# Kernel optimization log

Hardware: AMD Instinct MI355X
Metric: run time of the kernel (lower is better)

## Reference

```python
import jax, jax.numpy as jnp
import numpy as np

NEAR, FAR, N_SAMPLES = 1.0, 6.0, 64
FAR_APPEND = 1000.0


def setup_inputs() -> dict:
    key = jax.random.key(0)
    ks = jax.random.split(key, 8)
    B, R = 2, 4096
    # pixel coords in a 128x128 image
    x_pix = jax.random.uniform(ks[0], (B, R, 2), dtype=jnp.float32) * 128.0
    # plausible pinhole intrinsics (fx=fy=128, cx=cy=64)
    K = jnp.array([[128.0, 0.0, 64.0], [0.0, 128.0, 64.0], [0.0, 0.0, 1.0]], dtype=jnp.float32)
    intrinsics = jnp.tile(K[None], (B, 1, 1))
    # identity rotation, small translation cam2world
    c2w = jnp.eye(4, dtype=jnp.float32).at[:3, 3].set(jnp.array([0.1, -0.2, 0.5]))
    cam2world = jnp.tile(c2w[None], (B, 1, 1))
    H = 256
    W1 = jax.random.normal(ks[1], (3, H), dtype=jnp.float32) / np.sqrt(3.0)
    b1 = jnp.zeros((H,), jnp.float32)
    W2 = jax.random.normal(ks[2], (H, H), dtype=jnp.float32) / np.sqrt(H)
    b2 = jnp.zeros((H,), jnp.float32)
    W3 = jax.random.normal(ks[3], (H, 4), dtype=jnp.float32) / np.sqrt(H)
    b3 = jnp.zeros((4,), jnp.float32)
    return {"x_pix": x_pix, "intrinsics": intrinsics, "cam2world": cam2world,
            "W1": W1, "b1": b1, "W2": W2, "b2": b2, "W3": W3, "b3": b3}


def _radiance_field(pts, W1, b1, W2, b2, W3, b3):
    # pts: (B, N, 3) -> sigma (B, N, 1), rad (B, N, 3)
    h = jax.nn.relu(pts @ W1 + b1)
    h = jax.nn.relu(h @ W2 + b2)
    o = h @ W3 + b3
    return jax.nn.relu(o[..., :1]), jax.nn.sigmoid(o[..., 1:])


def _get_world_rays(x_pix, intrinsics, cam2world):
    B, R, _ = x_pix.shape
    inv_K = jnp.linalg.inv(intrinsics)  # (B,3,3)
    xy_hom = jnp.concatenate([x_pix, jnp.ones((B, R, 1), x_pix.dtype)], axis=-1)  # (B,R,3)
    dirs_cam = jnp.einsum("bij,brj->bri", inv_K, xy_hom)  # unnormalized cam-frame dirs
    dirs_hom = jnp.concatenate([dirs_cam, jnp.zeros((B, R, 1), x_pix.dtype)], axis=-1)  # w=0 vector
    dirs_world = jnp.einsum("bij,brj->bri", cam2world, dirs_hom)[..., :3]
    origins = jnp.broadcast_to(cam2world[:, None, :3, 3], (B, R, 3))
    return origins, dirs_world


def _volume_integral(z_vals, sigmas, radiances):
    # z_vals: (S,); sigmas: (B,R,S,1); radiances: (B,R,S,3)
    dists = jnp.diff(z_vals, append=jnp.array([FAR_APPEND], z_vals.dtype))  # (S,)
    alpha = 1.0 - jnp.exp(-sigmas * dists[None, None, :, None])  # (B,R,S,1)
    Ts = jnp.cumprod(1.0 - alpha, axis=2)  # inclusive cumprod, matching torch
    weights = alpha * Ts  # (B,R,S,1)
    rgb = jnp.sum(weights * radiances, axis=2)  # (B,R,3)
    depth_map = jnp.einsum("brsv,s->brv", weights, z_vals)  # (B,R,1)
    return rgb, depth_map, weights


def reference(x_pix, intrinsics, cam2world, W1, b1, W2, b2, W3, b3):
    B, R = x_pix.shape[0], x_pix.shape[1]
    ros, rds = _get_world_rays(x_pix, intrinsics, cam2world)
    z_vals = jnp.linspace(NEAR, FAR, N_SAMPLES, dtype=x_pix.dtype)  # (S,)
    pts = ros[:, :, None, :] + rds[:, :, None, :] * z_vals[None, None, :, None]  # (B,R,S,3)
    pts = pts.reshape(B, -1, 3)
    sigma, rad = _radiance_field(pts, W1, b1, W2, b2, W3, b3)
    sigma = sigma.reshape(B, R, N_SAMPLES, 1)
    rad = rad.reshape(B, R, N_SAMPLES, 3)
    rgb, depth_map, weights = _volume_integral(z_vals, sigma, rad)
    accum = jnp.sum(weights, axis=-2)  # (B,R,1)
    rgb = rgb + (1.0 - accum)  # white background
    return rgb, depth_map
```

## Files before the change

### kernel.cpp

```cpp
#include <hip/hip_runtime.h>

typedef unsigned short u16;
typedef _Float16 f16x8 __attribute__((ext_vector_type(8)));
typedef float    f32x4  __attribute__((ext_vector_type(4)));
typedef float    f32x16 __attribute__((ext_vector_type(16)));

#define NRAYS 8192

#define WS_W2T  0
#define WS_B2   131072
#define WS_W3   132096
#define WS_B3   136192
#define WS_W1   136208
#define WS_B1   139280
#define WS_INTR 140304
#define WS_C2W  140384

__device__ __forceinline__ float bf2f(u16 u){
  union { unsigned int i; float f; } v; v.i = ((unsigned int)u) << 16; return v.f;
}
__device__ __forceinline__ u16 f2h(float f){
  union { _Float16 h; u16 u; } v; v.h = (_Float16)f;
  return v.u;
}
__device__ __forceinline__ int detect_bf16(const void* intr){
  return (((const u16*)intr)[0] == 0x4300u) ? 1 : 0;
}

__device__ __forceinline__ void conv_arr(const void* src, float* dst, int n, int bf, int tid){
  if (bf){
    const u16* s = (const u16*)src;
    for (int i = tid; i < n; i += 256) dst[i] = bf2f(s[i]);
  } else {
    const float* s = (const float*)src;
    for (int i = tid; i < n; i += 256) dst[i] = s[i];
  }
}

__global__ void prep(const void* __restrict__ W2, const void* __restrict__ W1,
                     const void* __restrict__ b1, const void* __restrict__ b2,
                     const void* __restrict__ W3, const void* __restrict__ b3,
                     const void* __restrict__ intr, const void* __restrict__ c2w,
                     char* __restrict__ ws)
{
  const int bf = detect_bf16(intr);
  const int t = threadIdx.x;
  if (blockIdx.x == 16){
    conv_arr(W1,  (float*)(ws + WS_W1),  768,  bf, t);
    conv_arr(b1,  (float*)(ws + WS_B1),  256,  bf, t);
    conv_arr(b2,  (float*)(ws + WS_B2),  256,  bf, t);
    conv_arr(W3,  (float*)(ws + WS_W3),  1024, bf, t);
    conv_arr(b3,  (float*)(ws + WS_B3),  4,    bf, t);
    conv_arr(intr,(float*)(ws + WS_INTR),18,   bf, t);
    conv_arr(c2w, (float*)(ws + WS_C2W), 32,   bf, t);
    return;
  }
  __shared__ u16 tile[64][72];
  const int bx = blockIdx.x & 3;
  const int by = blockIdx.x >> 2;
  const int c = t & 63, rb = t >> 6;
  u16* W2T = (u16*)(ws + WS_W2T);
  #pragma unroll
  for (int rr = 0; rr < 64; rr += 4){
    int k = bx*64 + rr + rb;
    int n = by*64 + c;
    float v = bf ? bf2f(((const u16*)W2)[k*256 + n]) : ((const float*)W2)[k*256 + n];
    tile[rr + rb][c] = f2h(v);
  }
  __syncthreads();
  #pragma unroll
  for (int rr = 0; rr < 64; rr += 4){
    int n = by*64 + rr + rb;
    int k = bx*64 + c;
    W2T[n*256 + k] = tile[c][rr + rb];
  }
}

__global__ __launch_bounds__(256, 2) void nerf_fused(
    const void* __restrict__ x_pix,
    const void* __restrict__ intr,
    const char* __restrict__ ws,
    float* __restrict__ out)
{
  __shared__ __align__(16) u16   h1s[128 * 256];
  __shared__ __align__(16) float obuf[4 * 128 * 4];

  const int tid = threadIdx.x;
  const int l   = tid & 63;
  const int w   = tid >> 6;
  const int ray = w >> 1;
  const int rayg = blockIdx.x * 2 + ray;
  const int bb   = rayg >> 12;
  const int bf   = detect_bf16(intr);

  const float* intrf = (const float*)(ws + WS_INTR);
  const float* c2wf  = (const float*)(ws + WS_C2W);
  const float* W1f   = (const float*)(ws + WS_W1);
  const float* b1f   = (const float*)(ws + WS_B1);
  const float* b2f   = (const float*)(ws + WS_B2);
  const float* W3f   = (const float*)(ws + WS_W3);
  const u16*   W2T   = (const u16*)(ws + WS_W2T);

  float px, py;
  if (bf){
    px = bf2f(((const u16*)x_pix)[rayg*2 + 0]);
    py = bf2f(((const u16*)x_pix)[rayg*2 + 1]);
  } else {
    px = ((const float*)x_pix)[rayg*2 + 0];
    py = ((const float*)x_pix)[rayg*2 + 1];
  }
  float Ka[9], Mm[16];
  #pragma unroll
  for (int i = 0; i < 9;  i++) Ka[i] = intrf[bb*9  + i];
  #pragma unroll
  for (int i = 0; i < 16; i++) Mm[i] = c2wf[bb*16 + i];
  float a = Ka[0], b_ = Ka[1], c = Ka[2];
  float d = Ka[3], e  = Ka[4], f = Ka[5];
  float g = Ka[6], h_ = Ka[7], i9 = Ka[8];
  float det = a*(e*i9 - f*h_) - b_*(d*i9 - f*g) + c*(d*h_ - e*g);
  float inv = 1.0f / det;
  float i00 = (e*i9 - f*h_)*inv, i01 = (c*h_ - b_*i9)*inv, i02 = (b_*f - c*e)*inv;
  float i10 = (f*g - d*i9)*inv, i11 = (a*i9 - c*g)*inv, i12 = (c*d - a*f)*inv;
  float i20 = (d*h_ - e*g)*inv, i21 = (b_*g - a*h_)*inv, i22 = (a*e - b_*d)*inv;
  float dcx = i00*px + i01*py + i02;
  float dcy = i10*px + i11*py + i12;
  float dcz = i20*px + i21*py + i22;
  float dx = Mm[0]*dcx + Mm[1]*dcy + Mm[2]*dcz;
  float dy = Mm[4]*dcx + Mm[5]*dcy + Mm[6]*dcz;
  float dz = Mm[8]*dcx + Mm[9]*dcy + Mm[10]*dcz;
  float ox = Mm[3], oy = Mm[7], oz = Mm[11];

  const int kbase = (w & 1)*128 + l*2;
  float aa0, aa1, gg0, gg1;
  {
    float2 r0 = *(const float2*)(W1f + kbase);
    float2 r1 = *(const float2*)(W1f + 256 + kbase);
    float2 r2 = *(const float2*)(W1f + 512 + kbase);
    float2 rb = *(const float2*)(b1f + kbase);
    aa0 = ox*r0.x + oy*r1.x + oz*r2.x + rb.x;
    aa1 = ox*r0.y + oy*r1.y + oz*r2.y + rb.y;
    gg0 = dx*r0.x + dy*r1.x + dz*r2.x;
    gg1 = dx*r0.y + dy*r1.y + dz*r2.y;
  }
  const float step = 5.0f / 63.0f;
  const int chunk_w = ((w & 1) << 4) + (l >> 2);
  const int sub_b   = (l & 3) << 2;
  {
    char* hb = (char*)h1s + (ray*64)*512;
    #pragma unroll 8
    for (int s = 0; s < 64; s++){
      float z = 1.0f + step * (float)s;
      u16 e0 = f2h(fmaxf(fmaf(gg0, z, aa0), 0.0f));
      u16 e1 = f2h(fmaxf(fmaf(gg1, z, aa1), 0.0f));
      unsigned pk = (unsigned)e0 | ((unsigned)e1 << 16);
      *(unsigned*)(hb + s*512 + ((chunk_w ^ (s & 7)) << 4) + sub_b) = pk;
    }
  }
  __syncthreads();

  const int l31 = l & 31;
  const int h   = l >> 5;
  const int m7  = l31 & 7;
  const int nbase = w * 64;

  f32x16 acc[2][4];
  #pragma unroll
  for (int nt = 0; nt < 2; nt++)
    #pragma unroll
    for (int mt = 0; mt < 4; mt++)
      acc[nt][mt] = (f32x16){0.f,0.f,0.f,0.f,0.f,0.f,0.f,0.f,
                             0.f,0.f,0.f,0.f,0.f,0.f,0.f,0.f};

  const u16* Arow = W2T + (nbase + l31)*256 + h*8;
  const char* hbase = (const char*)h1s;

  f16x8 a_cur[2];
  a_cur[0] = *(const f16x8*)(Arow);
  a_cur[1] = *(const f16x8*)(Arow + 32*256);

  #pragma unroll
  for (int t = 0; t < 16; t++){
    f16x8 a_nxt[2];
    if (t < 15){
      a_nxt[0] = *(const f16x8*)(Arow + (t+1)*16);
      a_nxt[1] = *(const f16x8*)(Arow + 32*256 + (t+1)*16);
    }
    const int swz = ((2*t + h) ^ m7) << 4;
    f16x8 bfr[4];
    #pragma unroll
    for (int mt = 0; mt < 4; mt++)
      bfr[mt] = *(const f16x8*)(hbase + (mt*32 + l31)*512 + swz);
    #pragma unroll
    for (int nt = 0; nt < 2; nt++)
      #pragma unroll
      for (int mt = 0; mt < 4; mt++)
        acc[nt][mt] = __builtin_amdgcn_mfma_f32_32x32x16_f16(
            a_cur[nt], bfr[mt], acc[nt][mt], 0, 0, 0);
    if (t < 15){ a_cur[0] = a_nxt[0]; a_cur[1] = a_nxt[1]; }
  }

  f32x4 o_m[4];
  #pragma unroll
  for (int mt = 0; mt < 4; mt++) o_m[mt] = (f32x4){0.f,0.f,0.f,0.f};

  #pragma unroll
  for (int nt = 0; nt < 2; nt++){
    #pragma unroll
    for (int gq = 0; gq < 4; gq++){
      const int n0 = nbase + nt*32 + gq*8 + h*4;
      f32x4 b2v = *(const f32x4*)(b2f + n0);
      f32x4 w30 = *(const f32x4*)(W3f + n0*4);
      f32x4 w31 = *(const f32x4*)(W3f + (n0+1)*4);
      f32x4 w32 = *(const f32x4*)(W3f + (n0+2)*4);
      f32x4 w33 = *(const f32x4*)(W3f + (n0+3)*4);
      #pragma unroll
      for (int mt = 0; mt < 4; mt++){
        float h0 = fmaxf(acc[nt][mt][gq*4+0] + b2v.x, 0.0f);
        float h1 = fmaxf(acc[nt][mt][gq*4+1] + b2v.y, 0.0f);
        float h2 = fmaxf(acc[nt][mt][gq*4+2] + b2v.z, 0.0f);
        float h3 = fmaxf(acc[nt][mt][gq*4+3] + b2v.w, 0.0f);
        o_m[mt] = o_m[mt] + h0*w30 + h1*w31 + h2*w32 + h3*w33;
      }
    }
  }

  #pragma unroll
  for (int mt = 0; mt < 4; mt++)
    #pragma unroll
    for (int j = 0; j < 4; j++){
      float v = o_m[mt][j];
      v += __shfl_xor(v, 32, 64);
      o_m[mt][j] = v;
    }

  if (h == 0){
    #pragma unroll
    for (int mt = 0; mt < 4; mt++)
      *(f32x4*)&obuf[(w*128 + mt*32 + l31)*4] = o_m[mt];
  }
  __syncthreads();

  if (w < 2){
    const int m = w*64 + l;
    const f32x4* ob4 = (const f32x4*)obuf;
    f32x4 oj  = ob4[m] + ob4[128 + m] + ob4[256 + m] + ob4[384 + m];
    f32x4 b3v = *(const f32x4*)(ws + WS_B3);
    float o_s0 = oj.x + b3v.x;
    float o_s1 = oj.y + b3v.y;
    float o_s2 = oj.z + b3v.z;
    float o_s3 = oj.w + b3v.w;

    const float zc    = 1.0f + step * (float)l;
    const float znext = (l == 63) ? 1000.0f : (1.0f + step * (float)(l + 1));
    const float dist  = znext - zc;
    float sigma = fmaxf(o_s0, 0.0f);
    float alpha = 1.0f - __expf(-sigma * dist);
    float t = 1.0f - alpha;
    #pragma unroll
    for (int sh = 1; sh < 64; sh <<= 1){
      float u = __shfl_up(t, sh, 64);
      if (l >= sh) t *= u;
    }
    float wgt = alpha * t;
    float r0 = 1.0f / (1.0f + __expf(-o_s1));
    float r1 = 1.0f / (1.0f + __expf(-o_s2));
    float r2 = 1.0f / (1.0f + __expf(-o_s3));
    float s0 = wgt*r0, s1 = wgt*r1, s2 = wgt*r2, sw = wgt, sz = wgt*zc;
    #pragma unroll
    for (int sh = 1; sh < 64; sh <<= 1){
      s0 += __shfl_xor(s0, sh, 64);
      s1 += __shfl_xor(s1, sh, 64);
      s2 += __shfl_xor(s2, sh, 64);
      sw += __shfl_xor(sw, sh, 64);
      sz += __shfl_xor(sz, sh, 64);
    }
    if (l == 0){
      const int rg = blockIdx.x*2 + w;
      float bg = 1.0f - sw;
      out[rg*3 + 0] = s0 + bg;
      out[rg*3 + 1] = s1 + bg;
      out[rg*3 + 2] = s2 + bg;
      out[3*NRAYS + rg] = sz;
    }
  }
}

extern "C" void kernel_launch(void* const* d_in, const int* in_sizes, int n_in,
                              void* d_out, int out_size, void* d_ws, size_t ws_size,
                              hipStream_t stream)
{
  const void* x_pix = d_in[0];
  const void* intr  = d_in[1];
  const void* c2w   = d_in[2];
  const void* W1    = d_in[3];
  const void* b1    = d_in[4];
  const void* W2    = d_in[5];
  const void* b2    = d_in[6];
  const void* W3    = d_in[7];
  const void* b3    = d_in[8];
  float* outp = (float*)d_out;
  char*  ws   = (char*)d_ws;

  hipLaunchKernelGGL(prep, dim3(17), dim3(256), 0, stream,
                     W2, W1, b1, b2, W3, b3, intr, c2w, ws);
  hipLaunchKernelGGL(nerf_fused, dim3(NRAYS/2), dim3(256), 0, stream,
                     x_pix, intr, ws, outp);
}
```

Measured before the change: 175.7 us.

## Deepen W2 global prefetch, double-buffer LDS B fragments, stage b2/W3 in LDS

The W2T A-fragment prefetch becomes a three-deep rotating buffer instead of one step ahead, and the B fragments read from LDS are now loaded one k-step ahead. Both changes hide global and LDS latency behind the MFMA chain. b2 and W3 are loaded once per block, overlapping the layer-1 compute, and staged in shared memory so the epilogue reads LDS instead of global memory. The cost is higher register pressure, which could cause spills at launch_bounds(256,2), plus 5KB more LDS per block.

```diff
diff --git a/kernel.cpp b/kernel.cpp
--- a/kernel.cpp
+++ b/kernel.cpp
@@ -84,6 +84,7 @@
 {
   __shared__ __align__(16) u16   h1s[128 * 256];
   __shared__ __align__(16) float obuf[4 * 128 * 4];
+  __shared__ __align__(16) float cbuf[1280];
 
   const int tid = threadIdx.x;
   const int l   = tid & 63;
@@ -100,6 +101,12 @@
   const float* b2f   = (const float*)(ws + WS_B2);
   const float* W3f   = (const float*)(ws + WS_W3);
   const u16*   W2T   = (const u16*)(ws + WS_W2T);
+
+  float stg0 = b2f[tid];
+  float stg1 = W3f[tid];
+  float stg2 = W3f[tid + 256];
+  float stg3 = W3f[tid + 512];
+  float stg4 = W3f[tid + 768];
 
   float px, py;
   if (bf){
@@ -156,6 +163,12 @@
       *(unsigned*)(hb + s*512 + ((chunk_w ^ (s & 7)) << 4) + sub_b) = pk;
     }
   }
+
+  cbuf[tid]        = stg0;
+  cbuf[256 + tid]  = stg1;
+  cbuf[512 + tid]  = stg2;
+  cbuf[768 + tid]  = stg3;
+  cbuf[1024 + tid] = stg4;
   __syncthreads();
 
   const int l31 = l & 31;
@@ -174,29 +187,46 @@
   const u16* Arow = W2T + (nbase + l31)*256 + h*8;
   const char* hbase = (const char*)h1s;
 
-  f16x8 a_cur[2];
-  a_cur[0] = *(const f16x8*)(Arow);
-  a_cur[1] = *(const f16x8*)(Arow + 32*256);
+  f16x8 ap[3][2];
+  #pragma unroll
+  for (int pp = 0; pp < 3; pp++){
+    ap[pp][0] = *(const f16x8*)(Arow + pp*16);
+    ap[pp][1] = *(const f16x8*)(Arow + 32*256 + pp*16);
+  }
+  f16x8 bcur[4];
+  {
+    const int swz0 = ((0 + h) ^ m7) << 4;
+    #pragma unroll
+    for (int mt = 0; mt < 4; mt++)
+      bcur[mt] = *(const f16x8*)(hbase + (mt*32 + l31)*512 + swz0);
+  }
 
   #pragma unroll
   for (int t = 0; t < 16; t++){
-    f16x8 a_nxt[2];
+    const int sl = t % 3;
+    f16x8 a0 = ap[sl][0];
+    f16x8 a1 = ap[sl][1];
+    if (t + 3 < 16){
+      ap[sl][0] = *(const f16x8*)(Arow + (t+3)*16);
+      ap[sl][1] = *(const f16x8*)(Arow + 32*256 + (t+3)*16);
+    }
+    f16x8 bnxt[4];
     if (t < 15){
-      a_nxt[0] = *(const f16x8*)(Arow + (t+1)*16);
-      a_nxt[1] = *(const f16x8*)(Arow + 32*256 + (t+1)*16);
-    }
-    const int swz = ((2*t + h) ^ m7) << 4;
-    f16x8 bfr[4];
-    #pragma unroll
-    for (int mt = 0; mt < 4; mt++)
-      bfr[mt] = *(const f16x8*)(hbase + (mt*32 + l31)*512 + swz);
+      const int swzn = ((2*(t+1) + h) ^ m7) << 4;
+      #pragma unroll
+      for (int mt = 0; mt < 4; mt++)
+        bnxt[mt] = *(const f16x8*)(hbase + (mt*32 + l31)*512 + swzn);
+    }
     #pragma unroll
     for (int nt = 0; nt < 2; nt++)
       #pragma unroll
       for (int mt = 0; mt < 4; mt++)
         acc[nt][mt] = __builtin_amdgcn_mfma_f32_32x32x16_f16(
-            a_cur[nt], bfr[mt], acc[nt][mt], 0, 0, 0);
-    if (t < 15){ a_cur[0] = a_nxt[0]; a_cur[1] = a_nxt[1]; }
+            nt == 0 ? a0 : a1, bcur[mt], acc[nt][mt], 0, 0, 0);
+    if (t < 15){
+      #pragma unroll
+      for (int mt = 0; mt < 4; mt++) bcur[mt] = bnxt[mt];
+    }
   }
 
   f32x4 o_m[4];
@@ -208,11 +238,11 @@
     #pragma unroll
     for (int gq = 0; gq < 4; gq++){
       const int n0 = nbase + nt*32 + gq*8 + h*4;
-      f32x4 b2v = *(const f32x4*)(b2f + n0);
-      f32x4 w30 = *(const f32x4*)(W3f + n0*4);
-      f32x4 w31 = *(const f32x4*)(W3f + (n0+1)*4);
-      f32x4 w32 = *(const f32x4*)(W3f + (n0+2)*4);
-      f32x4 w33 = *(const f32x4*)(W3f + (n0+3)*4);
+      f32x4 b2v = *(const f32x4*)(cbuf + n0);
+      f32x4 w30 = *(const f32x4*)(cbuf + 256 + n0*4);
+      f32x4 w31 = *(const f32x4*)(cbuf + 256 + (n0+1)*4);
+      f32x4 w32 = *(const f32x4*)(cbuf + 256 + (n0+2)*4);
+      f32x4 w33 = *(const f32x4*)(cbuf + 256 + (n0+3)*4);
       #pragma unroll
       for (int mt = 0; mt < 4; mt++){
         float h0 = fmaxf(acc[nt][mt][gq*4+0] + b2v.x, 0.0f);
```

New measurement: 165.9 us. 1.06x faster.

## Split layer-2 GEMM across eight waves per block and stage W3/b2 in LDS

Applied to the files above, without the earlier changes.

The fused NeRF kernel goes from 256 to 512 threads per block. Each of the eight waves now computes a 32-column slice of the hidden layer, which halves per-wave accumulators and lets more waves overlap, and the layer-1 writes are split across half-waves by sample. b2 and W3 are staged in shared memory, and the partial outputs are reduced in two stages through obuf before two waves run the compositing tail. The prep kernel uses smaller 32x32 transpose tiles over 64 blocks. The cost is an extra barrier and a read-modify-write pass over the reduction buffer, plus launch bounds that may limit registers.

```diff
diff --git a/kernel.cpp b/kernel.cpp
--- a/kernel.cpp
+++ b/kernel.cpp
@@ -45,7 +45,7 @@
 {
   const int bf = detect_bf16(intr);
   const int t = threadIdx.x;
-  if (blockIdx.x == 16){
+  if (blockIdx.x == 64){
     conv_arr(W1,  (float*)(ws + WS_W1),  768,  bf, t);
     conv_arr(b1,  (float*)(ws + WS_B1),  256,  bf, t);
     conv_arr(b2,  (float*)(ws + WS_B2),  256,  bf, t);
@@ -55,28 +55,72 @@
     conv_arr(c2w, (float*)(ws + WS_C2W), 32,   bf, t);
     return;
   }
-  __shared__ u16 tile[64][72];
-  const int bx = blockIdx.x & 3;
-  const int by = blockIdx.x >> 2;
-  const int c = t & 63, rb = t >> 6;
+  __shared__ u16 tile[32][34];
+  const int bx = blockIdx.x & 7;
+  const int by = blockIdx.x >> 3;
+  const int c = t & 31, r = t >> 5;
   u16* W2T = (u16*)(ws + WS_W2T);
   #pragma unroll
-  for (int rr = 0; rr < 64; rr += 4){
-    int k = bx*64 + rr + rb;
-    int n = by*64 + c;
+  for (int rr = 0; rr < 32; rr += 8){
+    int k = bx*32 + rr + r;
+    int n = by*32 + c;
     float v = bf ? bf2f(((const u16*)W2)[k*256 + n]) : ((const float*)W2)[k*256 + n];
-    tile[rr + rb][c] = f2h(v);
+    tile[rr + r][c] = f2h(v);
   }
   __syncthreads();
   #pragma unroll
-  for (int rr = 0; rr < 64; rr += 4){
-    int n = by*64 + rr + rb;
-    int k = bx*64 + c;
-    W2T[n*256 + k] = tile[c][rr + rb];
-  }
-}
-
-__global__ __launch_bounds__(256, 2) void nerf_fused(
+  for (int rr = 0; rr < 32; rr += 8){
+    int n = by*32 + rr + r;
+    int k = bx*32 + c;
+    W2T[n*256 + k] = tile[c][rr + r];
+  }
+}
+
+__device__ __forceinline__ void do_tail(const float* ob, int mrow, int rg, int l,
+                                        f32x4 b3v, float* __restrict__ out)
+{
+  const float step = 5.0f / 63.0f;
+  const f32x4* ob4 = (const f32x4*)ob;
+  f32x4 oj = ob4[mrow] + ob4[128 + mrow] + ob4[256 + mrow] + ob4[384 + mrow];
+  float o_s0 = oj.x + b3v.x;
+  float o_s1 = oj.y + b3v.y;
+  float o_s2 = oj.z + b3v.z;
+  float o_s3 = oj.w + b3v.w;
+
+  const float zc    = 1.0f + step * (float)l;
+  const float znext = (l == 63) ? 1000.0f : (1.0f + step * (float)(l + 1));
+  const float dist  = znext - zc;
+  float sigma = fmaxf(o_s0, 0.0f);
+  float alpha = 1.0f - __expf(-sigma * dist);
+  float t = 1.0f - alpha;
+  #pragma unroll
+  for (int sh = 1; sh < 64; sh <<= 1){
+    float u = __shfl_up(t, sh, 64);
+    if (l >= sh) t *= u;
+  }
+  float wgt = alpha * t;
+  float q0 = 1.0f / (1.0f + __expf(-o_s1));
+  float q1 = 1.0f / (1.0f + __expf(-o_s2));
+  float q2 = 1.0f / (1.0f + __expf(-o_s3));
+  float s0 = wgt*q0, s1 = wgt*q1, s2 = wgt*q2, sw = wgt, sz = wgt*zc;
+  #pragma unroll
+  for (int sh = 1; sh < 64; sh <<= 1){
+    s0 += __shfl_xor(s0, sh, 64);
+    s1 += __shfl_xor(s1, sh, 64);
+    s2 += __shfl_xor(s2, sh, 64);
+    sw += __shfl_xor(sw, sh, 64);
+    sz += __shfl_xor(sz, sh, 64);
+  }
+  if (l == 0){
+    float bg = 1.0f - sw;
+    out[rg*3 + 0] = s0 + bg;
+    out[rg*3 + 1] = s1 + bg;
+    out[rg*3 + 2] = s2 + bg;
+    out[3*NRAYS + rg] = sz;
+  }
+}
+
+__global__ __launch_bounds__(512, 4) void nerf_fused(
     const void* __restrict__ x_pix,
     const void* __restrict__ intr,
     const char* __restrict__ ws,
@@ -84,14 +128,17 @@
 {
   __shared__ __align__(16) u16   h1s[128 * 256];
   __shared__ __align__(16) float obuf[4 * 128 * 4];
+  __shared__ __align__(16) float cbuf[1280];
 
   const int tid = threadIdx.x;
   const int l   = tid & 63;
   const int w   = tid >> 6;
-  const int ray = w >> 1;
-  const int rayg = blockIdx.x * 2 + ray;
-  const int bb   = rayg >> 12;
-  const int bf   = detect_bf16(intr);
+  const int rr  = w >> 2;
+  const int ks  = w & 3;
+  const int bf  = detect_bf16(intr);
+  const int ray0g = blockIdx.x * 2;
+  const int rayg  = ray0g + rr;
+  const int bb    = ray0g >> 12;
 
   const float* intrf = (const float*)(ws + WS_INTR);
   const float* c2wf  = (const float*)(ws + WS_C2W);
@@ -101,14 +148,10 @@
   const float* W3f   = (const float*)(ws + WS_W3);
   const u16*   W2T   = (const u16*)(ws + WS_W2T);
 
-  float px, py;
-  if (bf){
-    px = bf2f(((const u16*)x_pix)[rayg*2 + 0]);
-    py = bf2f(((const u16*)x_pix)[rayg*2 + 1]);
-  } else {
-    px = ((const float*)x_pix)[rayg*2 + 0];
-    py = ((const float*)x_pix)[rayg*2 + 1];
-  }
+  if (tid < 256) cbuf[tid] = b2f[tid];
+  cbuf[256 + tid]       = W3f[tid];
+  cbuf[256 + 512 + tid] = W3f[512 + tid];
+
   float Ka[9], Mm[16];
   #pragma unroll
   for (int i = 0; i < 9;  i++) Ka[i] = intrf[bb*9  + i];
@@ -122,105 +165,109 @@
   float i00 = (e*i9 - f*h_)*inv, i01 = (c*h_ - b_*i9)*inv, i02 = (b_*f - c*e)*inv;
   float i10 = (f*g - d*i9)*inv, i11 = (a*i9 - c*g)*inv, i12 = (c*d - a*f)*inv;
   float i20 = (d*h_ - e*g)*inv, i21 = (b_*g - a*h_)*inv, i22 = (a*e - b_*d)*inv;
-  float dcx = i00*px + i01*py + i02;
-  float dcy = i10*px + i11*py + i12;
-  float dcz = i20*px + i21*py + i22;
-  float dx = Mm[0]*dcx + Mm[1]*dcy + Mm[2]*dcz;
-  float dy = Mm[4]*dcx + Mm[5]*dcy + Mm[6]*dcz;
-  float dz = Mm[8]*dcx + Mm[9]*dcy + Mm[10]*dcz;
   float ox = Mm[3], oy = Mm[7], oz = Mm[11];
 
-  const int kbase = (w & 1)*128 + l*2;
-  float aa0, aa1, gg0, gg1;
+  const int kbase = ks*64 + (l & 31)*2;
+  const float2 w1r0 = *(const float2*)(W1f + kbase);
+  const float2 w1r1 = *(const float2*)(W1f + 256 + kbase);
+  const float2 w1r2 = *(const float2*)(W1f + 512 + kbase);
+  const float2 w1bb = *(const float2*)(b1f + kbase);
+  const float aa0 = ox*w1r0.x + oy*w1r1.x + oz*w1r2.x + w1bb.x;
+  const float aa1 = ox*w1r0.y + oy*w1r1.y + oz*w1r2.y + w1bb.y;
+
+  float px, py;
+  if (bf){
+    px = bf2f(((const u16*)x_pix)[rayg*2 + 0]);
+    py = bf2f(((const u16*)x_pix)[rayg*2 + 1]);
+  } else {
+    px = ((const float*)x_pix)[rayg*2 + 0];
+    py = ((const float*)x_pix)[rayg*2 + 1];
+  }
+  float gg0, gg1;
   {
-    float2 r0 = *(const float2*)(W1f + kbase);
-    float2 r1 = *(const float2*)(W1f + 256 + kbase);
-    float2 r2 = *(const float2*)(W1f + 512 + kbase);
-    float2 rb = *(const float2*)(b1f + kbase);
-    aa0 = ox*r0.x + oy*r1.x + oz*r2.x + rb.x;
-    aa1 = ox*r0.y + oy*r1.y + oz*r2.y + rb.y;
-    gg0 = dx*r0.x + dy*r1.x + dz*r2.x;
-    gg1 = dx*r0.y + dy*r1.y + dz*r2.y;
-  }
+    float dcx = i00*px + i01*py + i02;
+    float dcy = i10*px + i11*py + i12;
+    float dcz = i20*px + i21*py + i22;
+    float dx = Mm[0]*dcx + Mm[1]*dcy + Mm[2]*dcz;
+    float dy = Mm[4]*dcx + Mm[5]*dcy + Mm[6]*dcz;
+    float dz = Mm[8]*dcx + Mm[9]*dcy + Mm[10]*dcz;
+    gg0 = dx*w1r0.x + dy*w1r1.x + dz*w1r2.x;
+    gg1 = dx*w1r0.y + dy*w1r1.y + dz*w1r2.y;
+  }
+
   const float step = 5.0f / 63.0f;
-  const int chunk_w = ((w & 1) << 4) + (l >> 2);
+  const int chunk_w = ks*8 + ((l & 31) >> 2);
   const int sub_b   = (l & 3) << 2;
+  int off8[8];
+  #pragma unroll
+  for (int j = 0; j < 8; j++) off8[j] = ((chunk_w ^ j) << 4) + sub_b;
+
+  const int l31 = l & 31;
+  const int h   = l >> 5;
+  const int m7  = l31 & 7;
+  const int nbase = w * 32;
+  const u16* Arow = W2T + (nbase + l31)*256 + h*8;
+  const f32x4 b3v = *(const f32x4*)(ws + WS_B3);
+  const char* hP = (const char*)h1s;
+
   {
-    char* hb = (char*)h1s + (ray*64)*512;
+    char* hb = (char*)h1s + (rr*64)*512;
+    const int shalf = (l >> 5)*32;
     #pragma unroll 8
-    for (int s = 0; s < 64; s++){
+    for (int s2 = 0; s2 < 32; s2++){
+      const int s = shalf + s2;
       float z = 1.0f + step * (float)s;
       u16 e0 = f2h(fmaxf(fmaf(gg0, z, aa0), 0.0f));
       u16 e1 = f2h(fmaxf(fmaf(gg1, z, aa1), 0.0f));
-      unsigned pk = (unsigned)e0 | ((unsigned)e1 << 16);
-      *(unsigned*)(hb + s*512 + ((chunk_w ^ (s & 7)) << 4) + sub_b) = pk;
+      *(unsigned*)(hb + s*512 + off8[s & 7]) = (unsigned)e0 | ((unsigned)e1 << 16);
     }
   }
+
+  f16x8 ap[2];
+  ap[0] = *(const f16x8*)(Arow);
+  ap[1] = *(const f16x8*)(Arow + 16);
+
   __syncthreads();
 
-  const int l31 = l & 31;
-  const int h   = l >> 5;
-  const int m7  = l31 & 7;
-  const int nbase = w * 64;
-
-  f32x16 acc[2][4];
-  #pragma unroll
-  for (int nt = 0; nt < 2; nt++)
-    #pragma unroll
-    for (int mt = 0; mt < 4; mt++)
-      acc[nt][mt] = (f32x16){0.f,0.f,0.f,0.f,0.f,0.f,0.f,0.f,
-                             0.f,0.f,0.f,0.f,0.f,0.f,0.f,0.f};
-
-  const u16* Arow = W2T + (nbase + l31)*256 + h*8;
-  const char* hbase = (const char*)h1s;
-
-  f16x8 a_cur[2];
-  a_cur[0] = *(const f16x8*)(Arow);
-  a_cur[1] = *(const f16x8*)(Arow + 32*256);
+  f32x16 acc[4];
+  #pragma unroll
+  for (int mt = 0; mt < 4; mt++)
+    acc[mt] = (f32x16){0.f,0.f,0.f,0.f,0.f,0.f,0.f,0.f,
+                       0.f,0.f,0.f,0.f,0.f,0.f,0.f,0.f};
 
   #pragma unroll
   for (int t = 0; t < 16; t++){
-    f16x8 a_nxt[2];
-    if (t < 15){
-      a_nxt[0] = *(const f16x8*)(Arow + (t+1)*16);
-      a_nxt[1] = *(const f16x8*)(Arow + 32*256 + (t+1)*16);
-    }
+    f16x8 a0 = ap[t & 1];
+    if (t + 2 < 16)
+      ap[t & 1] = *(const f16x8*)(Arow + (t+2)*16);
     const int swz = ((2*t + h) ^ m7) << 4;
     f16x8 bfr[4];
     #pragma unroll
     for (int mt = 0; mt < 4; mt++)
-      bfr[mt] = *(const f16x8*)(hbase + (mt*32 + l31)*512 + swz);
-    #pragma unroll
-    for (int nt = 0; nt < 2; nt++)
-      #pragma unroll
-      for (int mt = 0; mt < 4; mt++)
-        acc[nt][mt] = __builtin_amdgcn_mfma_f32_32x32x16_f16(
-            a_cur[nt], bfr[mt], acc[nt][mt], 0, 0, 0);
-    if (t < 15){ a_cur[0] = a_nxt[0]; a_cur[1] = a_nxt[1]; }
+      bfr[mt] = *(const f16x8*)(hP + (mt*32 + l31)*512 + swz);
+    #pragma unroll
+    for (int mt = 0; mt < 4; mt++)
+      acc[mt] = __builtin_amdgcn_mfma_f32_32x32x16_f16(a0, bfr[mt], acc[mt], 0, 0, 0);
   }
 
   f32x4 o_m[4];
   #pragma unroll
   for (int mt = 0; mt < 4; mt++) o_m[mt] = (f32x4){0.f,0.f,0.f,0.f};
-
-  #pragma unroll
-  for (int nt = 0; nt < 2; nt++){
-    #pragma unroll
-    for (int gq = 0; gq < 4; gq++){
-      const int n0 = nbase + nt*32 + gq*8 + h*4;
-      f32x4 b2v = *(const f32x4*)(b2f + n0);
-      f32x4 w30 = *(const f32x4*)(W3f + n0*4);
-      f32x4 w31 = *(const f32x4*)(W3f + (n0+1)*4);
-      f32x4 w32 = *(const f32x4*)(W3f + (n0+2)*4);
-      f32x4 w33 = *(const f32x4*)(W3f + (n0+3)*4);
-      #pragma unroll
-      for (int mt = 0; mt < 4; mt++){
-        float h0 = fmaxf(acc[nt][mt][gq*4+0] + b2v.x, 0.0f);
-        float h1 = fmaxf(acc[nt][mt][gq*4+1] + b2v.y, 0.0f);
-        float h2 = fmaxf(acc[nt][mt][gq*4+2] + b2v.z, 0.0f);
-        float h3 = fmaxf(acc[nt][mt][gq*4+3] + b2v.w, 0.0f);
-        o_m[mt] = o_m[mt] + h0*w30 + h1*w31 + h2*w32 + h3*w33;
-      }
+  #pragma unroll
+  for (int gq = 0; gq < 4; gq++){
+    const int n0 = nbase + gq*8 + h*4;
+    f32x4 b2v = *(const f32x4*)(cbuf + n0);
+    f32x4 w30 = *(const f32x4*)(cbuf + 256 + n0*4);
+    f32x4 w31 = *(const f32x4*)(cbuf + 256 + (n0+1)*4);
+    f32x4 w32 = *(const f32x4*)(cbuf + 256 + (n0+2)*4);
+    f32x4 w33 = *(const f32x4*)(cbuf + 256 + (n0+3)*4);
+    #pragma unroll
+    for (int mt = 0; mt < 4; mt++){
+      float h0 = fmaxf(acc[mt][gq*4+0] + b2v.x, 0.0f);
+      float h1 = fmaxf(acc[mt][gq*4+1] + b2v.y, 0.0f);
+      float h2 = fmaxf(acc[mt][gq*4+2] + b2v.z, 0.0f);
+      float h3 = fmaxf(acc[mt][gq*4+3] + b2v.w, 0.0f);
+      o_m[mt] = o_m[mt] + h0*w30 + h1*w31 + h2*w32 + h3*w33;
     }
   }
 
@@ -233,56 +280,25 @@
       o_m[mt][j] = v;
     }
 
-  if (h == 0){
+  if (w < 4 && h == 0){
     #pragma unroll
     for (int mt = 0; mt < 4; mt++)
       *(f32x4*)&obuf[(w*128 + mt*32 + l31)*4] = o_m[mt];
   }
   __syncthreads();
 
-  if (w < 2){
-    const int m = w*64 + l;
-    const f32x4* ob4 = (const f32x4*)obuf;
-    f32x4 oj  = ob4[m] + ob4[128 + m] + ob4[256 + m] + ob4[384 + m];
-    f32x4 b3v = *(const f32x4*)(ws + WS_B3);
-    float o_s0 = oj.x + b3v.x;
-    float o_s1 = oj.y + b3v.y;
-    float o_s2 = oj.z + b3v.z;
-    float o_s3 = oj.w + b3v.w;
-
-    const float zc    = 1.0f + step * (float)l;
-    const float znext = (l == 63) ? 1000.0f : (1.0f + step * (float)(l + 1));
-    const float dist  = znext - zc;
-    float sigma = fmaxf(o_s0, 0.0f);
-    float alpha = 1.0f - __expf(-sigma * dist);
-    float t = 1.0f - alpha;
-    #pragma unroll
-    for (int sh = 1; sh < 64; sh <<= 1){
-      float u = __shfl_up(t, sh, 64);
-      if (l >= sh) t *= u;
+  if (w >= 4 && h == 0){
+    #pragma unroll
+    for (int mt = 0; mt < 4; mt++){
+      const int idx = ((w - 4)*128 + mt*32 + l31)*4;
+      f32x4 v = *(const f32x4*)&obuf[idx];
+      *(f32x4*)&obuf[idx] = v + o_m[mt];
     }
-    float wgt = alpha * t;
-    float r0 = 1.0f / (1.0f + __expf(-o_s1));
-    float r1 = 1.0f / (1.0f + __expf(-o_s2));
-    float r2 = 1.0f / (1.0f + __expf(-o_s3));
-    float s0 = wgt*r0, s1 = wgt*r1, s2 = wgt*r2, sw = wgt, sz = wgt*zc;
-    #pragma unroll
-    for (int sh = 1; sh < 64; sh <<= 1){
-      s0 += __shfl_xor(s0, sh, 64);
-      s1 += __shfl_xor(s1, sh, 64);
-      s2 += __shfl_xor(s2, sh, 64);
-      sw += __shfl_xor(sw, sh, 64);
-      sz += __shfl_xor(sz, sh, 64);
-    }
-    if (l == 0){
-      const int rg = blockIdx.x*2 + w;
-      float bg = 1.0f - sw;
-      out[rg*3 + 0] = s0 + bg;
-      out[rg*3 + 1] = s1 + bg;
-      out[rg*3 + 2] = s2 + bg;
-      out[3*NRAYS + rg] = sz;
-    }
-  }
+  }
+  __syncthreads();
+
+  if (w == 0) do_tail(obuf, l,      ray0g,     l, b3v, out);
+  if (w == 4) do_tail(obuf, 64 + l, ray0g + 1, l, b3v, out);
 }
 
 extern "C" void kernel_launch(void* const* d_in, const int* in_sizes, int n_in,
@@ -301,8 +317,8 @@
   float* outp = (float*)d_out;
   char*  ws   = (char*)d_ws;
 
-  hipLaunchKernelGGL(prep, dim3(17), dim3(256), 0, stream,
+  hipLaunchKernelGGL(prep, dim3(65), dim3(256), 0, stream,
                      W2, W1, b1, b2, W3, b3, intr, c2w, ws);
-  hipLaunchKernelGGL(nerf_fused, dim3(NRAYS/2), dim3(256), 0, stream,
+  hipLaunchKernelGGL(nerf_fused, dim3(NRAYS/2), dim3(512), 0, stream,
                      x_pix, intr, ws, outp);
 }
```

Result: faster. 165.9 us (-5.5%).
